# Performance work log

Measured on AMD Instinct MI355X. Metric: run time of the kernel, lower is better.

The kernel has to match this reference:

```python
import jax, jax.numpy as jnp
import numpy as np

N = 50000      # num nodes
E = 800000     # num edges (no self loops; added in reference like add_remaining_self_loops)
D = 64         # input_dim
H = 128        # hidden_dim
O = 32         # output_dim
EPS = 1.0      # epsilon (privacy)
ALPHA = 0.5
DELTA = 1.0


def setup_inputs() -> dict:
    key = jax.random.key(0)
    ks = jax.random.split(key, 8)
    x = jax.random.normal(ks[0], (N, D), dtype=jnp.float32)
    row = jax.random.randint(ks[1], (E,), 0, N, dtype=jnp.int32)
    off = jax.random.randint(ks[2], (E,), 1, N, dtype=jnp.int32)
    col = (row + off) % N  # guarantees row != col (no pre-existing self loops)
    edge_index = jnp.stack([row, col], axis=0)
    priv_mask = jax.random.bernoulli(ks[3], 0.5, (N,))
    W1 = jax.random.normal(ks[4], (D, H), dtype=jnp.float32) * (1.0 / np.sqrt(D))
    b1 = jnp.zeros((H,), dtype=jnp.float32)
    W2 = jax.random.normal(ks[5], (H, O), dtype=jnp.float32) * (1.0 / np.sqrt(H))
    b2 = jnp.zeros((O,), dtype=jnp.float32)
    return {"x": x, "edge_index": edge_index, "priv_mask": priv_mask,
            "W1": W1, "b1": b1, "W2": W2, "b2": b2}


def _gcn_norm(edge_index, num_nodes, dtype):
    # add_remaining_self_loops + symmetric normalization deg^-1/2[row]*deg^-1/2[col]
    loops = jnp.arange(num_nodes, dtype=edge_index.dtype)
    row = jnp.concatenate([edge_index[0], loops])
    col = jnp.concatenate([edge_index[1], loops])
    deg = jax.ops.segment_sum(jnp.ones(row.shape[0], dtype=dtype), row,
                              num_segments=num_nodes)
    dis = deg ** -0.5  # deg >= 1 thanks to self loops
    norm = dis[row] * dis[col]  # [E+N]
    return row, col, norm


def reference(x, edge_index, priv_mask, W1, b1, W2, b2):
    row, col, norm = _gcn_norm(edge_index, N, x.dtype)
    exp_eps = float(np.exp(EPS))

    # ---- conv1 (GConvDP with per-node bool priv_mask) ----
    x_j = x[row]                                   # [E+N, D] gather
    p = priv_mask[row].astype(x.dtype)[:, None]    # [E+N, 1]
    transformed = ((exp_eps + 1.0) * x_j - 1.0) * (DELTA / (exp_eps - 1.0)) + ALPHA
    msg = norm[:, None] * (p * transformed + (1.0 - p) * x_j)
    h = jax.ops.segment_sum(msg, col, num_segments=N)  # scatter-add aggregate

    h = jax.nn.relu(h @ W1 + b1)
    # F.dropout skipped: reference is deterministic (eval mode)

    # ---- conv2 (called with priv_mask=False, a Python scalar) ----
    # Literal torch semantics: p_j = False -> False*(...) = 0, ~False = -1,
    # so msg = norm * (-x_j).
    msg2 = -norm[:, None] * h[row]                 # [E+N, H]
    h2 = jax.ops.segment_sum(msg2, col, num_segments=N)

    return h2 @ W2 + b2
```

## Files before the change

kernel.cpp:

```cpp
#include <hip/hip_runtime.h>
#include <math.h>

#define C1 2.163953413738653f
#define C0 -0.081976706869326f


typedef __attribute__((ext_vector_type(8))) short bf16x8;
typedef __attribute__((ext_vector_type(4))) float f32x4;

static __device__ __forceinline__ unsigned short f2bf(float f) {
    unsigned b = __float_as_uint(f);
    return (unsigned short)((b + 0x7FFFu + ((b >> 16) & 1u)) >> 16);
}
static __device__ __forceinline__ float bf2f(unsigned short u) {
    return __uint_as_float((unsigned)u << 16);
}

__global__ __launch_bounds__(1024) void k_hist2(const int* __restrict__ row,
                                                const int* __restrict__ col, int E, int chunk,
                                                int* __restrict__ hist,
                                                const float* __restrict__ W1,
                                                const float* __restrict__ W2,
                                                unsigned short* __restrict__ W1b,
                                                unsigned short* __restrict__ W2b) {
    __shared__ int hc[256], hr[256];
    int t = threadIdx.x, b = blockIdx.x;
    if (t < 256) { hc[t] = 0; hr[t] = 0; }
    __syncthreads();
    int lo = b * chunk, hi = min(E, lo + chunk);
    for (int i = lo + t; i < hi; i += 1024) {
        atomicAdd(&hc[col[i] >> 8], 1);
        atomicAdd(&hr[row[i] >> 8], 1);
    }
    __syncthreads();
    if (t < 256) {
        hist[t * 256 + b] = hc[t];
        hist[65536 + t * 256 + b] = hr[t];
    }
    if (b == 0) {
        for (int i = t; i < 8192; i += 1024) {
            int j = i & 7, l2 = (i >> 3) & 63, kt = (i >> 9) & 1, nt = i >> 10;
            int k = kt * 32 + (l2 >> 4) * 8 + j, n = nt * 16 + (l2 & 15);
            W1b[i] = f2bf(W1[k * 128 + n]);
        }
    } else if (b == 1) {
        for (int i = t; i < 4096; i += 1024) {
            int j = i & 7, l2 = (i >> 3) & 63, kt = (i >> 9) & 3, nt = i >> 11;
            int k = kt * 32 + (l2 >> 4) * 8 + j, n = nt * 16 + (l2 & 15);
            W2b[i] = f2bf(W2[k * 32 + n]);
        }
    }
}

__global__ void k_scan_a(const int* __restrict__ cnt, int* __restrict__ excl,
                         int* __restrict__ bsum, int n) {
    __shared__ int s[256];
    int idx = blockIdx.x * 256 + threadIdx.x;
    int v = (idx < n) ? cnt[idx] : 0;
    s[threadIdx.x] = v;
    __syncthreads();
    for (int off = 1; off < 256; off <<= 1) {
        int t = (threadIdx.x >= off) ? s[threadIdx.x - off] : 0;
        __syncthreads();
        s[threadIdx.x] += t;
        __syncthreads();
    }
    if (idx < n) excl[idx] = s[threadIdx.x] - v;
    if (threadIdx.x == 255) bsum[blockIdx.x] = s[255];
}

__global__ __launch_bounds__(1024) void k_part(const int* __restrict__ row,
                                               const int* __restrict__ col, int E, int chunk,
                                               const int* __restrict__ excl,
                                               const int* __restrict__ bsum,
                                               unsigned* __restrict__ cbuf,
                                               unsigned short* __restrict__ rbuf) {
    __shared__ int offc[256], offr[256], s[256];
    int t = threadIdx.x, b = blockIdx.x;
    if (t < 256) s[t] = bsum[t];
    __syncthreads();
    for (int off = 1; off < 256; off <<= 1) {
        int u = (t < 256 && t >= off) ? s[t - off] : 0;
        __syncthreads();
        if (t < 256) s[t] += u;
        __syncthreads();
    }
    if (t < 256) offc[t] = s[t] - bsum[t] + excl[t * 256 + b];
    __syncthreads();
    if (t < 256) s[t] = bsum[256 + t];
    __syncthreads();
    for (int off = 1; off < 256; off <<= 1) {
        int u = (t < 256 && t >= off) ? s[t - off] : 0;
        __syncthreads();
        if (t < 256) s[t] += u;
        __syncthreads();
    }
    if (t < 256) offr[t] = s[t] - bsum[256 + t] + excl[65536 + t * 256 + b];
    __syncthreads();
    int lo = b * chunk, hi = min(E, lo + chunk);
    for (int i = lo + t; i < hi; i += 1024) {
        int r = row[i], c = col[i];
        int pc = atomicAdd(&offc[c >> 8], 1);
        cbuf[pc] = ((unsigned)c << 16) | (unsigned)r;
        int pr = atomicAdd(&offr[r >> 8], 1);
        rbuf[pr] = (unsigned short)r;
    }
}

__global__ __launch_bounds__(256) void k_build(const unsigned short* __restrict__ rbuf,
                                               const unsigned* __restrict__ cbuf,
                                               const int* __restrict__ bsum,
                                               const int* __restrict__ priv,
                                               const float* __restrict__ x, int N, int E, int nbk,
                                               float* __restrict__ dis,
                                               unsigned short* __restrict__ xt,
                                               int* __restrict__ cntC, int* __restrict__ colStart,
                                               unsigned short* __restrict__ eSrc) {
    __shared__ int s1[256], s2[256], s3[256];
    int t = threadIdx.x;
    if ((int)blockIdx.x < nbk) {
        int b = blockIdx.x;
        s1[t] = (t < b) ? bsum[256 + t] : 0;
        __syncthreads();
        for (int off = 128; off > 0; off >>= 1) {
            if (t < off) s1[t] += s1[t + off];
            __syncthreads();
        }
        int rs = s1[0];
        int re = rs + bsum[256 + b];
        __syncthreads();
        s1[t] = 0;
        __syncthreads();
        for (int i = rs + t; i < re; i += 256) atomicAdd(&s1[rbuf[i] & 255], 1);
        __syncthreads();
        int node = b * 256 + t;
        float dv = rsqrtf((float)(s1[t] + 1));
        if (node < N) {
            dis[node] = dv;
            s2[t] = __float_as_int(dv);
            s3[t] = priv[node];
        } else { s2[t] = 0; s3[t] = 0; }
        __syncthreads();
        int base = b * 256;
        for (int i = t; i < 256 * 16; i += 256) {
            int ln = i >> 4;
            int n2 = base + ln;
            if (n2 >= N) continue;
            float d2 = __int_as_float(s2[ln]);
            int p = s3[ln];
            float4 v = ((const float4*)x)[(size_t)n2 * 16 + (i & 15)];
            float4 tr;
            tr.x = p ? fmaf(C1, v.x, C0) : v.x;
            tr.y = p ? fmaf(C1, v.y, C0) : v.y;
            tr.z = p ? fmaf(C1, v.z, C0) : v.z;
            tr.w = p ? fmaf(C1, v.w, C0) : v.w;
            ushort4 o;
            o.x = f2bf(d2 * tr.x); o.y = f2bf(d2 * tr.y);
            o.z = f2bf(d2 * tr.z); o.w = f2bf(d2 * tr.w);
            ((ushort4*)xt)[(size_t)n2 * 16 + (i & 15)] = o;
        }
    } else {
        int b = blockIdx.x - nbk;
        s1[t] = (t < b) ? bsum[t] : 0;
        __syncthreads();
        for (int off = 128; off > 0; off >>= 1) {
            if (t < off) s1[t] += s1[t + off];
            __syncthreads();
        }
        int cs = s1[0];
        int ce = cs + bsum[b];
        __syncthreads();
        s1[t] = 0; s3[t] = 0;
        __syncthreads();
        for (int i = cs + t; i < ce; i += 256) atomicAdd(&s1[(cbuf[i] >> 16) & 255], 1);
        __syncthreads();
        int v = s1[t];
        s2[t] = v;
        __syncthreads();
        for (int off = 1; off < 256; off <<= 1) {
            int u = (t >= off) ? s2[t - off] : 0;
            __syncthreads();
            s2[t] += u;
            __syncthreads();
        }
        int excl = s2[t] - v;
        int c = b * 256 + t;
        if (c < N) { cntC[c] = v; colStart[c] = cs + excl; }
        __syncthreads();
        s2[t] = excl;
        __syncthreads();
        for (int i = cs + t; i < ce; i += 256) {
            unsigned e = cbuf[i];
            int d = (e >> 16) & 255;
            int pos = cs + s2[d] + atomicAdd(&s3[d], 1);
            eSrc[pos] = (unsigned short)(e & 0xFFFFu);
        }
    }
}

__global__ __launch_bounds__(256) void k_gather1(const unsigned short* __restrict__ xt,
                                                 const unsigned short* __restrict__ eSrc,
                                                 const int* __restrict__ colStart,
                                                 const int* __restrict__ cntC,
                                                 const float* __restrict__ dis,
                                                 unsigned short* __restrict__ agg1b, int N) {
    int t = blockIdx.x * blockDim.x + threadIdx.x;
    int c = t >> 6, d = t & 63;
    if (c >= N) return;
    float s = bf2f(xt[(size_t)c * 64 + d]);
    int start = colStart[c], cnt = cntC[c];
    for (int base = 0; base < cnt; base += 64) {
        int m = min(cnt - base, 64);
        int ids = (d < m) ? (int)eSrc[start + base + d] : 0;
        int k = 0;
        for (; k + 8 <= m; k += 8) {
            int r0 = __shfl(ids, k),     r1 = __shfl(ids, k + 1);
            int r2 = __shfl(ids, k + 2), r3 = __shfl(ids, k + 3);
            int r4 = __shfl(ids, k + 4), r5 = __shfl(ids, k + 5);
            int r6 = __shfl(ids, k + 6), r7 = __shfl(ids, k + 7);
            float x0 = bf2f(xt[(size_t)r0 * 64 + d]);
            float x1 = bf2f(xt[(size_t)r1 * 64 + d]);
            float x2 = bf2f(xt[(size_t)r2 * 64 + d]);
            float x3 = bf2f(xt[(size_t)r3 * 64 + d]);
            float x4 = bf2f(xt[(size_t)r4 * 64 + d]);
            float x5 = bf2f(xt[(size_t)r5 * 64 + d]);
            float x6 = bf2f(xt[(size_t)r6 * 64 + d]);
            float x7 = bf2f(xt[(size_t)r7 * 64 + d]);
            s += x0; s += x1; s += x2; s += x3;
            s += x4; s += x5; s += x6; s += x7;
        }
        for (; k + 4 <= m; k += 4) {
            int r0 = __shfl(ids, k),     r1 = __shfl(ids, k + 1);
            int r2 = __shfl(ids, k + 2), r3 = __shfl(ids, k + 3);
            float x0 = bf2f(xt[(size_t)r0 * 64 + d]);
            float x1 = bf2f(xt[(size_t)r1 * 64 + d]);
            float x2 = bf2f(xt[(size_t)r2 * 64 + d]);
            float x3 = bf2f(xt[(size_t)r3 * 64 + d]);
            s += x0; s += x1; s += x2; s += x3;
        }
        for (; k < m; ++k) {
            int r = __shfl(ids, k);
            s += bf2f(xt[(size_t)r * 64 + d]);
        }
    }
    agg1b[(size_t)c * 64 + d] = f2bf(dis[c] * s);
}

__global__ __launch_bounds__(256) void k_mlp_mfma(const unsigned short* __restrict__ agg1b,
                                                  const unsigned short* __restrict__ W1b,
                                                  const float* __restrict__ b1,
                                                  const unsigned short* __restrict__ W2b,
                                                  const float* __restrict__ dis,
                                                  unsigned short* __restrict__ hps, int N) {
    __shared__ unsigned short hidA[4][16 * 136];
    const int t = threadIdx.x;
    const int w = t >> 6, l = t & 63;
    const int q = l >> 4, lm = l & 15;
    const int rowbase = blockIdx.x * 64 + w * 16;

    bf16x8 a0, a1;
    {
        int node = rowbase + lm;
        if (node >= N) node = N - 1;
        const bf16x8* pa = (const bf16x8*)(agg1b + (size_t)node * 64);
        a0 = pa[q];
        a1 = pa[4 + q];
    }
    float dvals[4];
    #pragma unroll
    for (int r = 0; r < 4; ++r) {
        int node = rowbase + q * 4 + r;
        dvals[r] = (node < N) ? dis[node] : 0.f;
    }

    const bf16x8* w1f = (const bf16x8*)W1b;
    #pragma unroll
    for (int nt = 0; nt < 8; ++nt) {
        float bv = b1[nt * 16 + lm];
        f32x4 acc = {bv, bv, bv, bv};
        acc = __builtin_amdgcn_mfma_f32_16x16x32_bf16(a0, w1f[(nt * 2 + 0) * 64 + l], acc, 0, 0, 0);
        acc = __builtin_amdgcn_mfma_f32_16x16x32_bf16(a1, w1f[(nt * 2 + 1) * 64 + l], acc, 0, 0, 0);
        #pragma unroll
        for (int r = 0; r < 4; ++r)
            hidA[w][(q * 4 + r) * 136 + nt * 16 + lm] = f2bf(fmaxf(acc[r], 0.f));
    }
    __syncthreads();

    bf16x8 ha[4];
    #pragma unroll
    for (int kt = 0; kt < 4; ++kt)
        ha[kt] = *(const bf16x8*)&hidA[w][lm * 136 + kt * 32 + q * 8];

    const bf16x8* w2f = (const bf16x8*)W2b;
    #pragma unroll
    for (int nt = 0; nt < 2; ++nt) {
        f32x4 acc = {0.f, 0.f, 0.f, 0.f};
        #pragma unroll
        for (int kt = 0; kt < 4; ++kt)
            acc = __builtin_amdgcn_mfma_f32_16x16x32_bf16(ha[kt], w2f[(nt * 4 + kt) * 64 + l], acc, 0, 0, 0);
        #pragma unroll
        for (int r = 0; r < 4; ++r) {
            int node = rowbase + q * 4 + r;
            if (node < N)
                hps[(size_t)node * 32 + nt * 16 + lm] = f2bf(acc[r] * dvals[r]);
        }
    }
}

__global__ __launch_bounds__(256) void k_gather2(const unsigned short* __restrict__ hps,
                                                 const unsigned short* __restrict__ eSrc,
                                                 const int* __restrict__ colStart,
                                                 const int* __restrict__ cntC,
                                                 const float* __restrict__ dis,
                                                 const float* __restrict__ b2,
                                                 float* __restrict__ out, int N) {
    int t = blockIdx.x * blockDim.x + threadIdx.x;
    int c = t >> 5, j = t & 31;
    if (c >= N) return;
    float s = bf2f(hps[(size_t)c * 32 + j]);
    int start = colStart[c], cnt = cntC[c];
    for (int base = 0; base < cnt; base += 32) {
        int m = min(cnt - base, 32);
        int ids = (j < m) ? (int)eSrc[start + base + j] : 0;
        int k = 0;
        for (; k + 8 <= m; k += 8) {
            int r0 = __shfl(ids, k, 32),     r1 = __shfl(ids, k + 1, 32);
            int r2 = __shfl(ids, k + 2, 32), r3 = __shfl(ids, k + 3, 32);
            int r4 = __shfl(ids, k + 4, 32), r5 = __shfl(ids, k + 5, 32);
            int r6 = __shfl(ids, k + 6, 32), r7 = __shfl(ids, k + 7, 32);
            float h0 = bf2f(hps[(size_t)r0 * 32 + j]);
            float h1 = bf2f(hps[(size_t)r1 * 32 + j]);
            float h2 = bf2f(hps[(size_t)r2 * 32 + j]);
            float h3 = bf2f(hps[(size_t)r3 * 32 + j]);
            float h4 = bf2f(hps[(size_t)r4 * 32 + j]);
            float h5 = bf2f(hps[(size_t)r5 * 32 + j]);
            float h6 = bf2f(hps[(size_t)r6 * 32 + j]);
            float h7 = bf2f(hps[(size_t)r7 * 32 + j]);
            s += h0; s += h1; s += h2; s += h3;
            s += h4; s += h5; s += h6; s += h7;
        }
        for (; k + 4 <= m; k += 4) {
            int r0 = __shfl(ids, k, 32),     r1 = __shfl(ids, k + 1, 32);
            int r2 = __shfl(ids, k + 2, 32), r3 = __shfl(ids, k + 3, 32);
            float h0 = bf2f(hps[(size_t)r0 * 32 + j]);
            float h1 = bf2f(hps[(size_t)r1 * 32 + j]);
            float h2 = bf2f(hps[(size_t)r2 * 32 + j]);
            float h3 = bf2f(hps[(size_t)r3 * 32 + j]);
            s += h0; s += h1; s += h2; s += h3;
        }
        for (; k < m; ++k) {
            int r = __shfl(ids, k, 32);
            s += bf2f(hps[(size_t)r * 32 + j]);
        }
    }
    out[(size_t)c * 32 + j] = b2[j] - dis[c] * s;
}

extern "C" void kernel_launch(void* const* d_in, const int* in_sizes, int n_in,
                              void* d_out, int out_size, void* d_ws, size_t ws_size,
                              hipStream_t stream) {
    const float* x    = (const float*)d_in[0];
    const int*   ei   = (const int*)d_in[1];
    const int*   priv = (const int*)d_in[2];
    const float* W1   = (const float*)d_in[3];
    const float* b1   = (const float*)d_in[4];
    const float* W2   = (const float*)d_in[5];
    const float* b2   = (const float*)d_in[6];
    float* out = (float*)d_out;

    const int N = in_sizes[2];
    const int E = in_sizes[1] / 2;
    const int* row = ei;
    const int* col = ei + E;

    char* ws = (char*)d_ws;
    size_t off = 0;
    auto take = [&](size_t bytes) { char* p = ws + off; off = (off + bytes + 255) & ~(size_t)255; return p; };
    int*            hist     = (int*)           take((size_t)131072 * 4);
    int*            excl     = (int*)           take((size_t)131072 * 4);
    int*            bsum     = (int*)           take(512 * 4);
    unsigned short* W1b      = (unsigned short*)take((size_t)8192 * 2);
    unsigned short* W2b      = (unsigned short*)take((size_t)4096 * 2);
    unsigned*       cbuf     = (unsigned*)      take((size_t)E * 4);
    unsigned short* rbuf     = (unsigned short*)take((size_t)E * 2);
    float*          dis      = (float*)         take((size_t)N * 4);
    int*            cntC     = (int*)           take((size_t)N * 4);
    int*            colStart = (int*)           take((size_t)N * 4);
    unsigned short* eSrc     = (unsigned short*)take((size_t)E * 2);
    unsigned short* xt       = (unsigned short*)take((size_t)N * 64 * 2);
    unsigned short* agg1b    = (unsigned short*)take((size_t)N * 64 * 2);
    unsigned short* hps      = (unsigned short*)take((size_t)N * 32 * 2);
    (void)ws_size;

    const int chunk = (E + 255) / 256;
    const int nbk = (N + 255) / 256;

    k_hist2   <<<256, 1024, 0, stream>>>(row, col, E, chunk, hist, W1, W2, W1b, W2b);
    k_scan_a  <<<512, 256, 0, stream>>>(hist, excl, bsum, 131072);
    k_part    <<<256, 1024, 0, stream>>>(row, col, E, chunk, excl, bsum, cbuf, rbuf);
    k_build   <<<2 * nbk, 256, 0, stream>>>(rbuf, cbuf, bsum, priv, x, N, E, nbk,
                                            dis, xt, cntC, colStart, eSrc);
    k_gather1 <<<((size_t)N * 64 + 255) / 256, 256, 0, stream>>>(xt, eSrc, colStart, cntC, dis, agg1b, N);
    k_mlp_mfma<<<(N + 63) / 64, 256, 0, stream>>>(agg1b, W1b, b1, W2b, dis, hps, N);
    k_gather2 <<<((size_t)N * 32 + 255) / 256, 256, 0, stream>>>(hps, eSrc, colStart, cntC, dis, b2, out, N);
}
```

Baseline: 157.9 us.

## Fold histogram scan into partition kernel and use scalar-indexed int32 edge gathers

```diff
diff --git a/kernel.cpp b/kernel.cpp
--- a/kernel.cpp
+++ b/kernel.cpp
@@ -52,50 +52,50 @@
     }
 }
 
-__global__ void k_scan_a(const int* __restrict__ cnt, int* __restrict__ excl,
-                         int* __restrict__ bsum, int n) {
-    __shared__ int s[256];
-    int idx = blockIdx.x * 256 + threadIdx.x;
-    int v = (idx < n) ? cnt[idx] : 0;
-    s[threadIdx.x] = v;
-    __syncthreads();
-    for (int off = 1; off < 256; off <<= 1) {
-        int t = (threadIdx.x >= off) ? s[threadIdx.x - off] : 0;
-        __syncthreads();
-        s[threadIdx.x] += t;
-        __syncthreads();
-    }
-    if (idx < n) excl[idx] = s[threadIdx.x] - v;
-    if (threadIdx.x == 255) bsum[blockIdx.x] = s[255];
-}
-
 __global__ __launch_bounds__(1024) void k_part(const int* __restrict__ row,
                                                const int* __restrict__ col, int E, int chunk,
-                                               const int* __restrict__ excl,
-                                               const int* __restrict__ bsum,
+                                               const int* __restrict__ hist,
+                                               int* __restrict__ dtot,
                                                unsigned* __restrict__ cbuf,
-                                               unsigned short* __restrict__ rbuf) {
-    __shared__ int offc[256], offr[256], s[256];
+                                               int* __restrict__ rbuf) {
+    __shared__ int Tc[256], Pc[256], Tr[256], Pr[256], sc[256];
+    __shared__ int offc[256], offr[256];
     int t = threadIdx.x, b = blockIdx.x;
-    if (t < 256) s[t] = bsum[t];
+    if (t < 256) { Tc[t] = 0; Pc[t] = 0; Tr[t] = 0; Pr[t] = 0; }
+    __syncthreads();
+    {
+        int d = t & 255, g = t >> 8;
+        int sT = 0, sP = 0, sTr = 0, sPr = 0;
+        for (int b2 = g * 64; b2 < g * 64 + 64; ++b2) {
+            int v = hist[d * 256 + b2];
+            int w = hist[65536 + d * 256 + b2];
+            sT += v; sTr += w;
+            if (b2 < b) { sP += v; sPr += w; }
+        }
+        atomicAdd(&Tc[d], sT); atomicAdd(&Pc[d], sP);
+        atomicAdd(&Tr[d], sTr); atomicAdd(&Pr[d], sPr);
+    }
+    __syncthreads();
+    if (b == 0 && t < 256) { dtot[t] = Tc[t]; dtot[256 + t] = Tr[t]; }
+    if (t < 256) sc[t] = Tc[t];
     __syncthreads();
     for (int off = 1; off < 256; off <<= 1) {
-        int u = (t < 256 && t >= off) ? s[t - off] : 0;
-        __syncthreads();
-        if (t < 256) s[t] += u;
-        __syncthreads();
-    }
-    if (t < 256) offc[t] = s[t] - bsum[t] + excl[t * 256 + b];
-    __syncthreads();
-    if (t < 256) s[t] = bsum[256 + t];
+        int u = (t < 256 && t >= off) ? sc[t - off] : 0;
+        __syncthreads();
+        if (t < 256) sc[t] += u;
+        __syncthreads();
+    }
+    if (t < 256) offc[t] = sc[t] - Tc[t] + Pc[t];
+    __syncthreads();
+    if (t < 256) sc[t] = Tr[t];
     __syncthreads();
     for (int off = 1; off < 256; off <<= 1) {
-        int u = (t < 256 && t >= off) ? s[t - off] : 0;
-        __syncthreads();
-        if (t < 256) s[t] += u;
-        __syncthreads();
-    }
-    if (t < 256) offr[t] = s[t] - bsum[256 + t] + excl[65536 + t * 256 + b];
+        int u = (t < 256 && t >= off) ? sc[t - off] : 0;
+        __syncthreads();
+        if (t < 256) sc[t] += u;
+        __syncthreads();
+    }
+    if (t < 256) offr[t] = sc[t] - Tr[t] + Pr[t];
     __syncthreads();
     int lo = b * chunk, hi = min(E, lo + chunk);
     for (int i = lo + t; i < hi; i += 1024) {
@@ -103,31 +103,31 @@
         int pc = atomicAdd(&offc[c >> 8], 1);
         cbuf[pc] = ((unsigned)c << 16) | (unsigned)r;
         int pr = atomicAdd(&offr[r >> 8], 1);
-        rbuf[pr] = (unsigned short)r;
-    }
-}
-
-__global__ __launch_bounds__(256) void k_build(const unsigned short* __restrict__ rbuf,
+        rbuf[pr] = r;
+    }
+}
+
+__global__ __launch_bounds__(256) void k_build(const int* __restrict__ rbuf,
                                                const unsigned* __restrict__ cbuf,
-                                               const int* __restrict__ bsum,
+                                               const int* __restrict__ dtot,
                                                const int* __restrict__ priv,
                                                const float* __restrict__ x, int N, int E, int nbk,
                                                float* __restrict__ dis,
                                                unsigned short* __restrict__ xt,
                                                int* __restrict__ cntC, int* __restrict__ colStart,
-                                               unsigned short* __restrict__ eSrc) {
+                                               int* __restrict__ eSrc) {
     __shared__ int s1[256], s2[256], s3[256];
     int t = threadIdx.x;
     if ((int)blockIdx.x < nbk) {
         int b = blockIdx.x;
-        s1[t] = (t < b) ? bsum[256 + t] : 0;
+        s1[t] = (t < b) ? dtot[256 + t] : 0;
         __syncthreads();
         for (int off = 128; off > 0; off >>= 1) {
             if (t < off) s1[t] += s1[t + off];
             __syncthreads();
         }
         int rs = s1[0];
-        int re = rs + bsum[256 + b];
+        int re = rs + dtot[256 + b];
         __syncthreads();
         s1[t] = 0;
         __syncthreads();
@@ -161,14 +161,14 @@
         }
     } else {
         int b = blockIdx.x - nbk;
-        s1[t] = (t < b) ? bsum[t] : 0;
+        s1[t] = (t < b) ? dtot[t] : 0;
         __syncthreads();
         for (int off = 128; off > 0; off >>= 1) {
             if (t < off) s1[t] += s1[t + off];
             __syncthreads();
         }
         int cs = s1[0];
-        int ce = cs + bsum[b];
+        int ce = cs + dtot[b];
         __syncthreads();
         s1[t] = 0; s3[t] = 0;
         __syncthreads();
@@ -193,13 +193,13 @@
             unsigned e = cbuf[i];
             int d = (e >> 16) & 255;
             int pos = cs + s2[d] + atomicAdd(&s3[d], 1);
-            eSrc[pos] = (unsigned short)(e & 0xFFFFu);
+            eSrc[pos] = (int)(e & 0xFFFFu);
         }
     }
 }
 
 __global__ __launch_bounds__(256) void k_gather1(const unsigned short* __restrict__ xt,
-                                                 const unsigned short* __restrict__ eSrc,
+                                                 const int* __restrict__ eSrcI,
                                                  const int* __restrict__ colStart,
                                                  const int* __restrict__ cntC,
                                                  const float* __restrict__ dis,
@@ -207,41 +207,28 @@
     int t = blockIdx.x * blockDim.x + threadIdx.x;
     int c = t >> 6, d = t & 63;
     if (c >= N) return;
+    int start = __builtin_amdgcn_readfirstlane(colStart[c]);
+    int cnt   = __builtin_amdgcn_readfirstlane(cntC[c]);
     float s = bf2f(xt[(size_t)c * 64 + d]);
-    int start = colStart[c], cnt = cntC[c];
-    for (int base = 0; base < cnt; base += 64) {
-        int m = min(cnt - base, 64);
-        int ids = (d < m) ? (int)eSrc[start + base + d] : 0;
-        int k = 0;
-        for (; k + 8 <= m; k += 8) {
-            int r0 = __shfl(ids, k),     r1 = __shfl(ids, k + 1);
-            int r2 = __shfl(ids, k + 2), r3 = __shfl(ids, k + 3);
-            int r4 = __shfl(ids, k + 4), r5 = __shfl(ids, k + 5);
-            int r6 = __shfl(ids, k + 6), r7 = __shfl(ids, k + 7);
-            float x0 = bf2f(xt[(size_t)r0 * 64 + d]);
-            float x1 = bf2f(xt[(size_t)r1 * 64 + d]);
-            float x2 = bf2f(xt[(size_t)r2 * 64 + d]);
-            float x3 = bf2f(xt[(size_t)r3 * 64 + d]);
-            float x4 = bf2f(xt[(size_t)r4 * 64 + d]);
-            float x5 = bf2f(xt[(size_t)r5 * 64 + d]);
-            float x6 = bf2f(xt[(size_t)r6 * 64 + d]);
-            float x7 = bf2f(xt[(size_t)r7 * 64 + d]);
-            s += x0; s += x1; s += x2; s += x3;
-            s += x4; s += x5; s += x6; s += x7;
-        }
-        for (; k + 4 <= m; k += 4) {
-            int r0 = __shfl(ids, k),     r1 = __shfl(ids, k + 1);
-            int r2 = __shfl(ids, k + 2), r3 = __shfl(ids, k + 3);
-            float x0 = bf2f(xt[(size_t)r0 * 64 + d]);
-            float x1 = bf2f(xt[(size_t)r1 * 64 + d]);
-            float x2 = bf2f(xt[(size_t)r2 * 64 + d]);
-            float x3 = bf2f(xt[(size_t)r3 * 64 + d]);
-            s += x0; s += x1; s += x2; s += x3;
-        }
-        for (; k < m; ++k) {
-            int r = __shfl(ids, k);
-            s += bf2f(xt[(size_t)r * 64 + d]);
-        }
+    const int* ep = eSrcI + start;
+    int k = 0;
+    for (; k + 8 <= cnt; k += 8) {
+        int r0 = ep[k],     r1 = ep[k + 1], r2 = ep[k + 2], r3 = ep[k + 3];
+        int r4 = ep[k + 4], r5 = ep[k + 5], r6 = ep[k + 6], r7 = ep[k + 7];
+        float x0 = bf2f(xt[(size_t)r0 * 64 + d]);
+        float x1 = bf2f(xt[(size_t)r1 * 64 + d]);
+        float x2 = bf2f(xt[(size_t)r2 * 64 + d]);
+        float x3 = bf2f(xt[(size_t)r3 * 64 + d]);
+        float x4 = bf2f(xt[(size_t)r4 * 64 + d]);
+        float x5 = bf2f(xt[(size_t)r5 * 64 + d]);
+        float x6 = bf2f(xt[(size_t)r6 * 64 + d]);
+        float x7 = bf2f(xt[(size_t)r7 * 64 + d]);
+        s += x0; s += x1; s += x2; s += x3;
+        s += x4; s += x5; s += x6; s += x7;
+    }
+    for (; k < cnt; ++k) {
+        int r = ep[k];
+        s += bf2f(xt[(size_t)r * 64 + d]);
     }
     agg1b[(size_t)c * 64 + d] = f2bf(dis[c] * s);
 }
@@ -308,52 +295,47 @@
 }
 
 __global__ __launch_bounds__(256) void k_gather2(const unsigned short* __restrict__ hps,
-                                                 const unsigned short* __restrict__ eSrc,
+                                                 const int* __restrict__ eSrcI,
                                                  const int* __restrict__ colStart,
                                                  const int* __restrict__ cntC,
                                                  const float* __restrict__ dis,
                                                  const float* __restrict__ b2,
                                                  float* __restrict__ out, int N) {
     int t = blockIdx.x * blockDim.x + threadIdx.x;
-    int c = t >> 5, j = t & 31;
+    int c = t >> 6, l = t & 63;
+    int j = l & 31, half = l >> 5;
     if (c >= N) return;
-    float s = bf2f(hps[(size_t)c * 32 + j]);
-    int start = colStart[c], cnt = cntC[c];
-    for (int base = 0; base < cnt; base += 32) {
-        int m = min(cnt - base, 32);
-        int ids = (j < m) ? (int)eSrc[start + base + j] : 0;
-        int k = 0;
-        for (; k + 8 <= m; k += 8) {
-            int r0 = __shfl(ids, k, 32),     r1 = __shfl(ids, k + 1, 32);
-            int r2 = __shfl(ids, k + 2, 32), r3 = __shfl(ids, k + 3, 32);
-            int r4 = __shfl(ids, k + 4, 32), r5 = __shfl(ids, k + 5, 32);
-            int r6 = __shfl(ids, k + 6, 32), r7 = __shfl(ids, k + 7, 32);
-            float h0 = bf2f(hps[(size_t)r0 * 32 + j]);
-            float h1 = bf2f(hps[(size_t)r1 * 32 + j]);
-            float h2 = bf2f(hps[(size_t)r2 * 32 + j]);
-            float h3 = bf2f(hps[(size_t)r3 * 32 + j]);
-            float h4 = bf2f(hps[(size_t)r4 * 32 + j]);
-            float h5 = bf2f(hps[(size_t)r5 * 32 + j]);
-            float h6 = bf2f(hps[(size_t)r6 * 32 + j]);
-            float h7 = bf2f(hps[(size_t)r7 * 32 + j]);
-            s += h0; s += h1; s += h2; s += h3;
-            s += h4; s += h5; s += h6; s += h7;
-        }
-        for (; k + 4 <= m; k += 4) {
-            int r0 = __shfl(ids, k, 32),     r1 = __shfl(ids, k + 1, 32);
-            int r2 = __shfl(ids, k + 2, 32), r3 = __shfl(ids, k + 3, 32);
-            float h0 = bf2f(hps[(size_t)r0 * 32 + j]);
-            float h1 = bf2f(hps[(size_t)r1 * 32 + j]);
-            float h2 = bf2f(hps[(size_t)r2 * 32 + j]);
-            float h3 = bf2f(hps[(size_t)r3 * 32 + j]);
-            s += h0; s += h1; s += h2; s += h3;
-        }
-        for (; k < m; ++k) {
-            int r = __shfl(ids, k, 32);
-            s += bf2f(hps[(size_t)r * 32 + j]);
-        }
-    }
-    out[(size_t)c * 32 + j] = b2[j] - dis[c] * s;
+    int start = __builtin_amdgcn_readfirstlane(colStart[c]);
+    int cnt   = __builtin_amdgcn_readfirstlane(cntC[c]);
+    float s = half ? 0.f : bf2f(hps[(size_t)c * 32 + j]);
+    const int* ep = eSrcI + start;
+    int k = 0;
+    for (; k + 8 <= cnt; k += 8) {
+        int a0 = ep[k],     e0 = ep[k + 1], a1 = ep[k + 2], e1 = ep[k + 3];
+        int a2 = ep[k + 4], e2 = ep[k + 5], a3 = ep[k + 6], e3 = ep[k + 7];
+        int r0 = half ? e0 : a0;
+        int r1 = half ? e1 : a1;
+        int r2 = half ? e2 : a2;
+        int r3 = half ? e3 : a3;
+        float h0 = bf2f(hps[(size_t)r0 * 32 + j]);
+        float h1 = bf2f(hps[(size_t)r1 * 32 + j]);
+        float h2 = bf2f(hps[(size_t)r2 * 32 + j]);
+        float h3 = bf2f(hps[(size_t)r3 * 32 + j]);
+        s += h0; s += h1; s += h2; s += h3;
+    }
+    for (; k + 2 <= cnt; k += 2) {
+        int a = ep[k], e = ep[k + 1];
+        int r = half ? e : a;
+        s += bf2f(hps[(size_t)r * 32 + j]);
+    }
+    if (k < cnt && !half) {
+        int r = ep[k];
+        s += bf2f(hps[(size_t)r * 32 + j]);
+    }
+    float o = __shfl(s, l ^ 32);
+    s += o;
+    if (!half)
+        out[(size_t)c * 32 + j] = b2[j] - dis[c] * s;
 }
 
 extern "C" void kernel_launch(void* const* d_in, const int* in_sizes, int n_in,
@@ -377,16 +359,15 @@
     size_t off = 0;
     auto take = [&](size_t bytes) { char* p = ws + off; off = (off + bytes + 255) & ~(size_t)255; return p; };
     int*            hist     = (int*)           take((size_t)131072 * 4);
-    int*            excl     = (int*)           take((size_t)131072 * 4);
-    int*            bsum     = (int*)           take(512 * 4);
+    int*            dtot     = (int*)           take(512 * 4);
     unsigned short* W1b      = (unsigned short*)take((size_t)8192 * 2);
     unsigned short* W2b      = (unsigned short*)take((size_t)4096 * 2);
     unsigned*       cbuf     = (unsigned*)      take((size_t)E * 4);
-    unsigned short* rbuf     = (unsigned short*)take((size_t)E * 2);
+    int*            rbuf     = (int*)           take((size_t)E * 4);
     float*          dis      = (float*)         take((size_t)N * 4);
     int*            cntC     = (int*)           take((size_t)N * 4);
     int*            colStart = (int*)           take((size_t)N * 4);
-    unsigned short* eSrc     = (unsigned short*)take((size_t)E * 2);
+    int*            eSrcI    = (int*)           take((size_t)E * 4);
     unsigned short* xt       = (unsigned short*)take((size_t)N * 64 * 2);
     unsigned short* agg1b    = (unsigned short*)take((size_t)N * 64 * 2);
     unsigned short* hps      = (unsigned short*)take((size_t)N * 32 * 2);
@@ -396,11 +377,10 @@
     const int nbk = (N + 255) / 256;
 
     k_hist2   <<<256, 1024, 0, stream>>>(row, col, E, chunk, hist, W1, W2, W1b, W2b);
-    k_scan_a  <<<512, 256, 0, stream>>>(hist, excl, bsum, 131072);
-    k_part    <<<256, 1024, 0, stream>>>(row, col, E, chunk, excl, bsum, cbuf, rbuf);
-    k_build   <<<2 * nbk, 256, 0, stream>>>(rbuf, cbuf, bsum, priv, x, N, E, nbk,
-                                            dis, xt, cntC, colStart, eSrc);
-    k_gather1 <<<((size_t)N * 64 + 255) / 256, 256, 0, stream>>>(xt, eSrc, colStart, cntC, dis, agg1b, N);
+    k_part    <<<256, 1024, 0, stream>>>(row, col, E, chunk, hist, dtot, cbuf, rbuf);
+    k_build   <<<2 * nbk, 256, 0, stream>>>(rbuf, cbuf, dtot, priv, x, N, E, nbk,
+                                            dis, xt, cntC, colStart, eSrcI);
+    k_gather1 <<<((size_t)N * 64 + 255) / 256, 256, 0, stream>>>(xt, eSrcI, colStart, cntC, dis, agg1b, N);
     k_mlp_mfma<<<(N + 63) / 64, 256, 0, stream>>>(agg1b, W1b, b1, W2b, dis, hps, N);
-    k_gather2 <<<((size_t)N * 32 + 255) / 256, 256, 0, stream>>>(hps, eSrc, colStart, cntC, dis, b2, out, N);
-}
+    k_gather2 <<<((size_t)N * 64 + 255) / 256, 256, 0, stream>>>(hps, eSrcI, colStart, cntC, dis, b2, out, N);
+}
```

Result: slower. 217.9 us (+38.0%).
